# Kernel optimization log

Measured on AMD Instinct MI355X. Metric: run time of the kernel, lower is better.

Reference implementation:

```python
import jax, jax.numpy as jnp
import numpy as np

B, H, S, D = 16, 12, 1024, 64  # batch, heads, seq, head_dim (dim=768, num_head=12)


def setup_inputs() -> dict:
    key = jax.random.key(0)
    ks = jax.random.split(key, 9)
    sc = 1.0 / np.sqrt(D)
    return {
        "x": jax.random.normal(ks[0], (B, H, S, D), dtype=jnp.float32),
        "Wq": jax.random.normal(ks[1], (D, D), dtype=jnp.float32) * sc,
        "bq": jax.random.normal(ks[2], (D,), dtype=jnp.float32) * 0.02,
        "Wk": jax.random.normal(ks[3], (D, D), dtype=jnp.float32) * sc,
        "bk": jax.random.normal(ks[4], (D,), dtype=jnp.float32) * 0.02,
        "Wv": jax.random.normal(ks[5], (D, D), dtype=jnp.float32) * sc,
        "bv": jax.random.normal(ks[6], (D,), dtype=jnp.float32) * 0.02,
        "Wo": jax.random.normal(ks[7], (D, D), dtype=jnp.float32) * sc,
        "bo": jax.random.normal(ks[8], (D,), dtype=jnp.float32) * 0.02,
    }


def reference(x, Wq, bq, Wk, bk, Wv, bv, Wo, bo):
    # torch Linear: y = x @ W^T + b, applied to last dim (head_dim)
    q = jnp.einsum("bhsd,ed->bhse", x, Wq) + bq
    k = jnp.einsum("bhsd,ed->bhse", x, Wk) + bk
    v = jnp.einsum("bhsd,ed->bhse", x, Wv) + bv
    scores = jnp.einsum("bhqd,bhkd->bhqk", q, k) / jnp.sqrt(jnp.float32(q.shape[-1]))
    attn = jax.nn.softmax(scores, axis=-1)
    out = jnp.einsum("bhqk,bhkd->bhqd", attn, v)
    out = jnp.einsum("bhsd,ed->bhse", out, Wo) + bo
    return out
```

## Files before the change

kernel.cpp:

```cpp
#include <hip/hip_runtime.h>
#include <math.h>


typedef __bf16 bf16x8 __attribute__((ext_vector_type(8)));
typedef float  f32x4  __attribute__((ext_vector_type(4)));

#define MFMA(a, b, c) __builtin_amdgcn_mfma_f32_16x16x32_bf16((a), (b), (c), 0, 0, 0)

static constexpr int S = 1024;
static constexpr int PAD = 72;
static constexpr size_t NE = 196608ull * 64ull;
static constexpr float QSCALE = 0.125f * 1.4426950408889634f;

__device__ inline unsigned long long pack4bf(float a, float b, float c, float d) {
    union { __bf16 h[4]; unsigned long long u; } pk;
    pk.h[0] = (__bf16)a; pk.h[1] = (__bf16)b; pk.h[2] = (__bf16)c; pk.h[3] = (__bf16)d;
    return pk.u;
}

union frag_u { bf16x8 v; unsigned long long u[2]; };

__global__ void prep(const float* __restrict__ x,
                     const float* __restrict__ Wq, const float* __restrict__ Wk,
                     const float* __restrict__ Wv, const float* __restrict__ Wo,
                     __bf16* __restrict__ xb,
                     __bf16* __restrict__ wqb, __bf16* __restrict__ wkb,
                     __bf16* __restrict__ wvb, __bf16* __restrict__ wob)
{
    const int bid = blockIdx.x;
    if (bid < 6144) {
        size_t p = ((size_t)bid * 256 + threadIdx.x) * 8;
        float4 a = *(const float4*)(x + p);
        float4 b = *(const float4*)(x + p + 4);
        union { unsigned long long u64[2]; uint4 v; } pk;
        pk.u64[0] = pack4bf(a.x, a.y, a.z, a.w);
        pk.u64[1] = pack4bf(b.x, b.y, b.z, b.w);
        *(uint4*)(xb + p) = pk.v;
    } else {
        const int wb  = bid - 6144;
        const int grp = wb >> 2;
        const int p   = (((wb & 3) * 256) + threadIdx.x) * 4;
        if (grp == 3) {
            int e = p >> 6, s = p & 63;
            int h = s >> 5, qp = (s >> 3) & 3, tb = (s >> 2) & 1;
            int d0 = 32 * h + 16 * tb + 4 * qp;
            float4 v = *(const float4*)(Wo + e * 64 + d0);
            *(unsigned long long*)(wob + p) = pack4bf(v.x, v.y, v.z, v.w);
        } else {
            const float* src = (grp == 0) ? Wq : (grp == 1) ? Wk : Wv;
            __bf16*      dst = (grp == 0) ? wqb : (grp == 1) ? wkb : wvb;
            float4 v = *(const float4*)(src + p);
            *(unsigned long long*)(dst + p) = pack4bf(v.x, v.y, v.z, v.w);
        }
    }
}

__global__ __launch_bounds__(256, 2) void attn(
    const __bf16* __restrict__ xb,
    const __bf16* __restrict__ wqb, const __bf16* __restrict__ wkb,
    const __bf16* __restrict__ wvb, const __bf16* __restrict__ wob,
    const float* __restrict__ bq, const float* __restrict__ bk,
    const float* __restrict__ bv, const float* __restrict__ bo,
    float* __restrict__ out)
{
    __shared__ __align__(16) union {
        __bf16 xq[256][PAD];
        struct {
            __bf16 w[2][64][PAD];
            __bf16 k[64][PAD];
            __bf16 v[64][PAD];
            __bf16 xk[64][PAD];
        } m;
    } L;

    const int tid = threadIdx.x;
    const int w = tid >> 6, lane = tid & 63, m = lane & 15, quad = lane >> 4;
    const int bh = blockIdx.x;
    const int q0 = blockIdx.y * 256 + w * 64;

    const __bf16* xqbase = xb + ((size_t)bh * 1024 + blockIdx.y * 256) * 64;
    #pragma unroll
    for (int i = tid * 8, it = 0; it < 8; i += 2048, it++) {
        int r = i >> 6, c = i & 63;
        *(uint4*)&L.xq[r][c] = *(const uint4*)(xqbase + i);
    }
    __syncthreads();
    bf16x8 xqf[4][2];
    #pragma unroll
    for (int g = 0; g < 4; g++) {
        xqf[g][0] = *(const bf16x8*)&L.xq[w * 64 + g * 16 + m][quad * 8];
        xqf[g][1] = *(const bf16x8*)&L.xq[w * 64 + g * 16 + m][32 + quad * 8];
    }
    __syncthreads();
    #pragma unroll
    for (int et = 0; et < 4; et++) {
        bf16x8 wf0 = *(const bf16x8*)(wqb + (size_t)(et * 16 + m) * 64 + quad * 8);
        bf16x8 wf1 = *(const bf16x8*)(wqb + (size_t)(et * 16 + m) * 64 + 32 + quad * 8);
        float4 bias = *(const float4*)(bq + et * 16 + quad * 4);
        #pragma unroll
        for (int g = 0; g < 4; g++) {
            f32x4 acc = {0.f, 0.f, 0.f, 0.f};
            acc = MFMA(wf0, xqf[g][0], acc);
            acc = MFMA(wf1, xqf[g][1], acc);
            *(unsigned long long*)&L.xq[w * 64 + g * 16 + m][et * 16 + quad * 4] =
                pack4bf((acc[0] + bias.x) * QSCALE, (acc[1] + bias.y) * QSCALE,
                        (acc[2] + bias.z) * QSCALE, (acc[3] + bias.w) * QSCALE);
        }
    }
    __syncthreads();
    bf16x8 qf[4][2];
    #pragma unroll
    for (int g = 0; g < 4; g++) {
        qf[g][0] = *(const bf16x8*)&L.xq[w * 64 + g * 16 + m][quad * 8];
        qf[g][1] = *(const bf16x8*)&L.xq[w * 64 + g * 16 + m][32 + quad * 8];
    }
    __syncthreads();

    #pragma unroll
    for (int i = tid * 8, it = 0; it < 2; i += 2048, it++) {
        int r = i >> 6, c = i & 63;
        *(uint4*)&L.m.w[0][r][c] = *(const uint4*)(wkb + i);
        *(uint4*)&L.m.w[1][r][c] = *(const uint4*)(wvb + i);
    }
    float4 bkr[4];
    float  bvr[4];
    #pragma unroll
    for (int et = 0; et < 4; et++) {
        bkr[et] = *(const float4*)(bk + et * 16 + quad * 4);
        bvr[et] = bv[et * 16 + m];
    }

    f32x4 o[4][4];
    float lsum[4] = {0.f, 0.f, 0.f, 0.f};
    #pragma unroll
    for (int g = 0; g < 4; g++)
        #pragma unroll
        for (int n = 0; n < 4; n++) o[g][n] = {0.f, 0.f, 0.f, 0.f};

    const __bf16* xkey = xb + (size_t)bh * 1024 * 64;
    uint4 px0 = *(const uint4*)(xkey + tid * 8);
    uint4 px1 = *(const uint4*)(xkey + 2048 + tid * 8);

    const int p0 = 32 * (w >> 1) + 8 * quad + 4 * (w & 1);

    for (int kb = 0; kb < 16; kb++) {
        __syncthreads();
        {
            int i0 = tid * 8;
            int i1 = i0 + 2048;
            *(uint4*)&L.m.xk[i0 >> 6][i0 & 63] = px0;
            *(uint4*)&L.m.xk[i1 >> 6][i1 & 63] = px1;
        }
        __syncthreads();
        {
            bf16x8 xk0 = *(const bf16x8*)&L.m.xk[w * 16 + m][quad * 8];
            bf16x8 xk1 = *(const bf16x8*)&L.m.xk[w * 16 + m][32 + quad * 8];
            #pragma unroll
            for (int et = 0; et < 4; et++) {
                bf16x8 kw0 = *(const bf16x8*)&L.m.w[0][et * 16 + m][quad * 8];
                bf16x8 kw1 = *(const bf16x8*)&L.m.w[0][et * 16 + m][32 + quad * 8];
                f32x4 ka = {0.f, 0.f, 0.f, 0.f};
                ka = MFMA(kw0, xk0, ka);
                ka = MFMA(kw1, xk1, ka);
                *(unsigned long long*)&L.m.k[w * 16 + m][et * 16 + quad * 4] =
                    pack4bf(ka[0] + bkr[et].x, ka[1] + bkr[et].y,
                            ka[2] + bkr[et].z, ka[3] + bkr[et].w);
                bf16x8 vw0 = *(const bf16x8*)&L.m.w[1][et * 16 + m][quad * 8];
                bf16x8 vw1 = *(const bf16x8*)&L.m.w[1][et * 16 + m][32 + quad * 8];
                f32x4 va = {0.f, 0.f, 0.f, 0.f};
                va = MFMA(xk0, vw0, va);
                va = MFMA(xk1, vw1, va);
                *(unsigned long long*)&L.m.v[et * 16 + m][p0] =
                    pack4bf(va[0] + bvr[et], va[1] + bvr[et],
                            va[2] + bvr[et], va[3] + bvr[et]);
            }
        }
        if (kb < 15) {
            const __bf16* xn = xkey + (kb + 1) * 4096;
            px0 = *(const uint4*)(xn + tid * 8);
            px1 = *(const uint4*)(xn + 2048 + tid * 8);
        }
        __syncthreads();
        #pragma unroll
        for (int gp = 0; gp < 2; gp++) {
            frag_u pb[2][2];
            #pragma unroll
            for (int t = 0; t < 4; t++) {
                bf16x8 ka0 = *(const bf16x8*)&L.m.k[t * 16 + m][quad * 8];
                bf16x8 ka1 = *(const bf16x8*)&L.m.k[t * 16 + m][32 + quad * 8];
                #pragma unroll
                for (int gl = 0; gl < 2; gl++) {
                    const int g = gp * 2 + gl;
                    f32x4 acc = {0.f, 0.f, 0.f, 0.f};
                    acc = MFMA(ka0, qf[g][0], acc);
                    acc = MFMA(ka1, qf[g][1], acc);
                    float e0 = __builtin_amdgcn_exp2f(acc[0]);
                    float e1 = __builtin_amdgcn_exp2f(acc[1]);
                    float e2 = __builtin_amdgcn_exp2f(acc[2]);
                    float e3 = __builtin_amdgcn_exp2f(acc[3]);
                    lsum[g] += (e0 + e1) + (e2 + e3);
                    pb[gl][t >> 1].u[t & 1] = pack4bf(e0, e1, e2, e3);
                }
            }
            #pragma unroll
            for (int n = 0; n < 4; n++) {
                bf16x8 va0 = *(const bf16x8*)&L.m.v[n * 16 + m][quad * 8];
                bf16x8 va1 = *(const bf16x8*)&L.m.v[n * 16 + m][32 + quad * 8];
                #pragma unroll
                for (int gl = 0; gl < 2; gl++) {
                    const int g = gp * 2 + gl;
                    o[g][n] = MFMA(va0, pb[gl][0].v, o[g][n]);
                    o[g][n] = MFMA(va1, pb[gl][1].v, o[g][n]);
                }
            }
        }
    }

    #pragma unroll
    for (int g = 0; g < 4; g++) {
        lsum[g] += __shfl_xor(lsum[g], 16);
        lsum[g] += __shfl_xor(lsum[g], 32);
    }

    bf16x8 wf[4][2];
    #pragma unroll
    for (int et = 0; et < 4; et++) {
        wf[et][0] = *(const bf16x8*)(wob + (size_t)(et * 16 + m) * 64 + quad * 8);
        wf[et][1] = *(const bf16x8*)(wob + (size_t)(et * 16 + m) * 64 + 32 + quad * 8);
    }
    float biasr[4];
    #pragma unroll
    for (int et = 0; et < 4; et++) biasr[et] = bo[et * 16 + m];

    #pragma unroll
    for (int g = 0; g < 4; g++) {
        const float inv = 1.f / lsum[g];
        frag_u af0, af1;
        af0.u[0] = pack4bf(o[g][0][0] * inv, o[g][0][1] * inv, o[g][0][2] * inv, o[g][0][3] * inv);
        af0.u[1] = pack4bf(o[g][1][0] * inv, o[g][1][1] * inv, o[g][1][2] * inv, o[g][1][3] * inv);
        af1.u[0] = pack4bf(o[g][2][0] * inv, o[g][2][1] * inv, o[g][2][2] * inv, o[g][2][3] * inv);
        af1.u[1] = pack4bf(o[g][3][0] * inv, o[g][3][1] * inv, o[g][3][2] * inv, o[g][3][3] * inv);
        #pragma unroll
        for (int et = 0; et < 4; et++) {
            f32x4 acc = {0.f, 0.f, 0.f, 0.f};
            acc = MFMA(af0.v, wf[et][0], acc);
            acc = MFMA(af1.v, wf[et][1], acc);
            #pragma unroll
            for (int r = 0; r < 4; r++) {
                size_t row = (size_t)bh * S + q0 + g * 16 + quad * 4 + r;
                out[row * 64 + et * 16 + m] = acc[r] + biasr[et];
            }
        }
    }
}

extern "C" void kernel_launch(void* const* d_in, const int* in_sizes, int n_in,
                              void* d_out, int out_size, void* d_ws, size_t ws_size,
                              hipStream_t stream) {
    const float* x  = (const float*)d_in[0];
    const float* Wq = (const float*)d_in[1];
    const float* bq = (const float*)d_in[2];
    const float* Wk = (const float*)d_in[3];
    const float* bk = (const float*)d_in[4];
    const float* Wv = (const float*)d_in[5];
    const float* bv = (const float*)d_in[6];
    const float* Wo = (const float*)d_in[7];
    const float* bo = (const float*)d_in[8];
    float* out = (float*)d_out;

    __bf16* xb  = (__bf16*)d_ws;
    __bf16* wob = xb + NE;
    __bf16* wqb = wob + 4096;
    __bf16* wkb = wqb + 4096;
    __bf16* wvb = wkb + 4096;

    prep<<<6160, 256, 0, stream>>>(x, Wq, Wk, Wv, Wo, xb, wqb, wkb, wvb, wob);
    attn<<<dim3(192, 4), 256, 0, stream>>>(xb, wqb, wkb, wvb, wob,
                                           bq, bk, bv, bo, out);
}
```

Before: 195.9 us.

## Fuse fp32-to-bf16 conversion into attention kernel and drop prep pass

Removes the separate prep kernel that converted x and the weights to bf16 in workspace; the attention kernel now reads fp32 inputs directly and packs to bf16 in registers. Key-block x rows are loaded straight into MFMA fragments instead of via an LDS staging buffer with register prefetch, which frees LDS and one barrier per iteration. Launch bounds are raised to allow 4 blocks per CU. The cost is doubled global read bytes for x (fp32, re-read by 4 query blocks) and the loss of the explicit next-block prefetch overlap.

```diff
diff --git a/kernel.cpp b/kernel.cpp
--- a/kernel.cpp
+++ b/kernel.cpp
@@ -9,7 +9,6 @@
 
 static constexpr int S = 1024;
 static constexpr int PAD = 72;
-static constexpr size_t NE = 196608ull * 64ull;
 static constexpr float QSCALE = 0.125f * 1.4426950408889634f;
 
 __device__ inline unsigned long long pack4bf(float a, float b, float c, float d) {
@@ -20,47 +19,12 @@
 
 union frag_u { bf16x8 v; unsigned long long u[2]; };
 
-__global__ void prep(const float* __restrict__ x,
-                     const float* __restrict__ Wq, const float* __restrict__ Wk,
-                     const float* __restrict__ Wv, const float* __restrict__ Wo,
-                     __bf16* __restrict__ xb,
-                     __bf16* __restrict__ wqb, __bf16* __restrict__ wkb,
-                     __bf16* __restrict__ wvb, __bf16* __restrict__ wob)
-{
-    const int bid = blockIdx.x;
-    if (bid < 6144) {
-        size_t p = ((size_t)bid * 256 + threadIdx.x) * 8;
-        float4 a = *(const float4*)(x + p);
-        float4 b = *(const float4*)(x + p + 4);
-        union { unsigned long long u64[2]; uint4 v; } pk;
-        pk.u64[0] = pack4bf(a.x, a.y, a.z, a.w);
-        pk.u64[1] = pack4bf(b.x, b.y, b.z, b.w);
-        *(uint4*)(xb + p) = pk.v;
-    } else {
-        const int wb  = bid - 6144;
-        const int grp = wb >> 2;
-        const int p   = (((wb & 3) * 256) + threadIdx.x) * 4;
-        if (grp == 3) {
-            int e = p >> 6, s = p & 63;
-            int h = s >> 5, qp = (s >> 3) & 3, tb = (s >> 2) & 1;
-            int d0 = 32 * h + 16 * tb + 4 * qp;
-            float4 v = *(const float4*)(Wo + e * 64 + d0);
-            *(unsigned long long*)(wob + p) = pack4bf(v.x, v.y, v.z, v.w);
-        } else {
-            const float* src = (grp == 0) ? Wq : (grp == 1) ? Wk : Wv;
-            __bf16*      dst = (grp == 0) ? wqb : (grp == 1) ? wkb : wvb;
-            float4 v = *(const float4*)(src + p);
-            *(unsigned long long*)(dst + p) = pack4bf(v.x, v.y, v.z, v.w);
-        }
-    }
-}
-
-__global__ __launch_bounds__(256, 2) void attn(
-    const __bf16* __restrict__ xb,
-    const __bf16* __restrict__ wqb, const __bf16* __restrict__ wkb,
-    const __bf16* __restrict__ wvb, const __bf16* __restrict__ wob,
-    const float* __restrict__ bq, const float* __restrict__ bk,
-    const float* __restrict__ bv, const float* __restrict__ bo,
+__global__ __launch_bounds__(256, 4) void attn(
+    const float* __restrict__ x,
+    const float* __restrict__ Wq, const float* __restrict__ bq,
+    const float* __restrict__ Wk, const float* __restrict__ bk,
+    const float* __restrict__ Wv, const float* __restrict__ bv,
+    const float* __restrict__ Wo, const float* __restrict__ bo,
     float* __restrict__ out)
 {
     __shared__ __align__(16) union {
@@ -69,7 +33,6 @@
             __bf16 w[2][64][PAD];
             __bf16 k[64][PAD];
             __bf16 v[64][PAD];
-            __bf16 xk[64][PAD];
         } m;
     } L;
 
@@ -78,11 +41,12 @@
     const int bh = blockIdx.x;
     const int q0 = blockIdx.y * 256 + w * 64;
 
-    const __bf16* xqbase = xb + ((size_t)bh * 1024 + blockIdx.y * 256) * 64;
-    #pragma unroll
-    for (int i = tid * 8, it = 0; it < 8; i += 2048, it++) {
+    const float* xq32 = x + ((size_t)bh * 1024 + blockIdx.y * 256) * 64;
+    #pragma unroll
+    for (int i = tid * 4; i < 16384; i += 1024) {
+        float4 v = *(const float4*)(xq32 + i);
         int r = i >> 6, c = i & 63;
-        *(uint4*)&L.xq[r][c] = *(const uint4*)(xqbase + i);
+        *(unsigned long long*)&L.xq[r][c] = pack4bf(v.x, v.y, v.z, v.w);
     }
     __syncthreads();
     bf16x8 xqf[4][2];
@@ -92,16 +56,25 @@
         xqf[g][1] = *(const bf16x8*)&L.xq[w * 64 + g * 16 + m][32 + quad * 8];
     }
     __syncthreads();
+
     #pragma unroll
     for (int et = 0; et < 4; et++) {
-        bf16x8 wf0 = *(const bf16x8*)(wqb + (size_t)(et * 16 + m) * 64 + quad * 8);
-        bf16x8 wf1 = *(const bf16x8*)(wqb + (size_t)(et * 16 + m) * 64 + 32 + quad * 8);
+        const float* wqrow = Wq + (size_t)(et * 16 + m) * 64;
+        float4 a0 = *(const float4*)(wqrow + quad * 8);
+        float4 a1 = *(const float4*)(wqrow + quad * 8 + 4);
+        float4 a2 = *(const float4*)(wqrow + 32 + quad * 8);
+        float4 a3 = *(const float4*)(wqrow + 36 + quad * 8);
+        frag_u wf0, wf1;
+        wf0.u[0] = pack4bf(a0.x, a0.y, a0.z, a0.w);
+        wf0.u[1] = pack4bf(a1.x, a1.y, a1.z, a1.w);
+        wf1.u[0] = pack4bf(a2.x, a2.y, a2.z, a2.w);
+        wf1.u[1] = pack4bf(a3.x, a3.y, a3.z, a3.w);
         float4 bias = *(const float4*)(bq + et * 16 + quad * 4);
         #pragma unroll
         for (int g = 0; g < 4; g++) {
             f32x4 acc = {0.f, 0.f, 0.f, 0.f};
-            acc = MFMA(wf0, xqf[g][0], acc);
-            acc = MFMA(wf1, xqf[g][1], acc);
+            acc = MFMA(wf0.v, xqf[g][0], acc);
+            acc = MFMA(wf1.v, xqf[g][1], acc);
             *(unsigned long long*)&L.xq[w * 64 + g * 16 + m][et * 16 + quad * 4] =
                 pack4bf((acc[0] + bias.x) * QSCALE, (acc[1] + bias.y) * QSCALE,
                         (acc[2] + bias.z) * QSCALE, (acc[3] + bias.w) * QSCALE);
@@ -117,10 +90,12 @@
     __syncthreads();
 
     #pragma unroll
-    for (int i = tid * 8, it = 0; it < 2; i += 2048, it++) {
+    for (int i = tid * 4; i < 4096; i += 1024) {
         int r = i >> 6, c = i & 63;
-        *(uint4*)&L.m.w[0][r][c] = *(const uint4*)(wkb + i);
-        *(uint4*)&L.m.w[1][r][c] = *(const uint4*)(wvb + i);
+        float4 a = *(const float4*)(Wk + i);
+        *(unsigned long long*)&L.m.w[0][r][c] = pack4bf(a.x, a.y, a.z, a.w);
+        float4 b = *(const float4*)(Wv + i);
+        *(unsigned long long*)&L.m.w[1][r][c] = pack4bf(b.x, b.y, b.z, b.w);
     }
     float4 bkr[4];
     float  bvr[4];
@@ -137,48 +112,41 @@
         #pragma unroll
         for (int n = 0; n < 4; n++) o[g][n] = {0.f, 0.f, 0.f, 0.f};
 
-    const __bf16* xkey = xb + (size_t)bh * 1024 * 64;
-    uint4 px0 = *(const uint4*)(xkey + tid * 8);
-    uint4 px1 = *(const uint4*)(xkey + 2048 + tid * 8);
-
+    const float* xk32 = x + (size_t)bh * 1024 * 64;
     const int p0 = 32 * (w >> 1) + 8 * quad + 4 * (w & 1);
 
     for (int kb = 0; kb < 16; kb++) {
         __syncthreads();
         {
-            int i0 = tid * 8;
-            int i1 = i0 + 2048;
-            *(uint4*)&L.m.xk[i0 >> 6][i0 & 63] = px0;
-            *(uint4*)&L.m.xk[i1 >> 6][i1 & 63] = px1;
-        }
-        __syncthreads();
-        {
-            bf16x8 xk0 = *(const bf16x8*)&L.m.xk[w * 16 + m][quad * 8];
-            bf16x8 xk1 = *(const bf16x8*)&L.m.xk[w * 16 + m][32 + quad * 8];
+            const float* xrow = xk32 + (size_t)(kb * 64 + w * 16 + m) * 64;
+            float4 a0 = *(const float4*)(xrow + quad * 8);
+            float4 a1 = *(const float4*)(xrow + quad * 8 + 4);
+            float4 a2 = *(const float4*)(xrow + 32 + quad * 8);
+            float4 a3 = *(const float4*)(xrow + 36 + quad * 8);
+            frag_u xk0, xk1;
+            xk0.u[0] = pack4bf(a0.x, a0.y, a0.z, a0.w);
+            xk0.u[1] = pack4bf(a1.x, a1.y, a1.z, a1.w);
+            xk1.u[0] = pack4bf(a2.x, a2.y, a2.z, a2.w);
+            xk1.u[1] = pack4bf(a3.x, a3.y, a3.z, a3.w);
             #pragma unroll
             for (int et = 0; et < 4; et++) {
                 bf16x8 kw0 = *(const bf16x8*)&L.m.w[0][et * 16 + m][quad * 8];
                 bf16x8 kw1 = *(const bf16x8*)&L.m.w[0][et * 16 + m][32 + quad * 8];
                 f32x4 ka = {0.f, 0.f, 0.f, 0.f};
-                ka = MFMA(kw0, xk0, ka);
-                ka = MFMA(kw1, xk1, ka);
+                ka = MFMA(kw0, xk0.v, ka);
+                ka = MFMA(kw1, xk1.v, ka);
                 *(unsigned long long*)&L.m.k[w * 16 + m][et * 16 + quad * 4] =
                     pack4bf(ka[0] + bkr[et].x, ka[1] + bkr[et].y,
                             ka[2] + bkr[et].z, ka[3] + bkr[et].w);
                 bf16x8 vw0 = *(const bf16x8*)&L.m.w[1][et * 16 + m][quad * 8];
                 bf16x8 vw1 = *(const bf16x8*)&L.m.w[1][et * 16 + m][32 + quad * 8];
                 f32x4 va = {0.f, 0.f, 0.f, 0.f};
-                va = MFMA(xk0, vw0, va);
-                va = MFMA(xk1, vw1, va);
+                va = MFMA(xk0.v, vw0, va);
+                va = MFMA(xk1.v, vw1, va);
                 *(unsigned long long*)&L.m.v[et * 16 + m][p0] =
                     pack4bf(va[0] + bvr[et], va[1] + bvr[et],
                             va[2] + bvr[et], va[3] + bvr[et]);
             }
-        }
-        if (kb < 15) {
-            const __bf16* xn = xkey + (kb + 1) * 4096;
-            px0 = *(const uint4*)(xn + tid * 8);
-            px1 = *(const uint4*)(xn + 2048 + tid * 8);
         }
         __syncthreads();
         #pragma unroll
@@ -225,8 +193,18 @@
     bf16x8 wf[4][2];
     #pragma unroll
     for (int et = 0; et < 4; et++) {
-        wf[et][0] = *(const bf16x8*)(wob + (size_t)(et * 16 + m) * 64 + quad * 8);
-        wf[et][1] = *(const bf16x8*)(wob + (size_t)(et * 16 + m) * 64 + 32 + quad * 8);
+        const float* worow = Wo + (size_t)(et * 16 + m) * 64;
+        float4 c0 = *(const float4*)(worow + 4 * quad);
+        float4 c1 = *(const float4*)(worow + 16 + 4 * quad);
+        float4 c2 = *(const float4*)(worow + 32 + 4 * quad);
+        float4 c3 = *(const float4*)(worow + 48 + 4 * quad);
+        frag_u f0, f1;
+        f0.u[0] = pack4bf(c0.x, c0.y, c0.z, c0.w);
+        f0.u[1] = pack4bf(c1.x, c1.y, c1.z, c1.w);
+        f1.u[0] = pack4bf(c2.x, c2.y, c2.z, c2.w);
+        f1.u[1] = pack4bf(c3.x, c3.y, c3.z, c3.w);
+        wf[et][0] = f0.v;
+        wf[et][1] = f1.v;
     }
     float biasr[4];
     #pragma unroll
@@ -268,13 +246,5 @@
     const float* bo = (const float*)d_in[8];
     float* out = (float*)d_out;
 
-    __bf16* xb  = (__bf16*)d_ws;
-    __bf16* wob = xb + NE;
-    __bf16* wqb = wob + 4096;
-    __bf16* wkb = wqb + 4096;
-    __bf16* wvb = wkb + 4096;
-
-    prep<<<6160, 256, 0, stream>>>(x, Wq, Wk, Wv, Wo, xb, wqb, wkb, wvb, wob);
-    attn<<<dim3(192, 4), 256, 0, stream>>>(xb, wqb, wkb, wvb, wob,
-                                           bq, bk, bv, bo, out);
+    attn<<<dim3(192, 4), 256, 0, stream>>>(x, Wq, bq, Wk, bk, Wv, bv, Wo, bo, out);
 }
```

Result: slower. 423.0 us (+115.9%).

## Load key-block x fragments directly into registers and pre-swizzle K/V weights

Applied to the files above, without the earlier changes.

Drops the LDS staging of each 64-row x key block. Each lane now loads its MFMA fragment straight from global memory, prefetched one block ahead, which removes one barrier per iteration. The K/V weights are stored once in a fragment-ordered LDS layout so each lane reads them contiguously, and two prologue barriers are removed. The attention MFMA section is also wrapped in s_setprio to favour compute waves. The cost is more scattered global loads per lane and a separate LDS array that is no longer unioned with the Q buffer.

```diff
diff --git a/kernel.cpp b/kernel.cpp
--- a/kernel.cpp
+++ b/kernel.cpp
@@ -66,12 +66,11 @@
     __shared__ __align__(16) union {
         __bf16 xq[256][PAD];
         struct {
-            __bf16 w[2][64][PAD];
             __bf16 k[64][PAD];
             __bf16 v[64][PAD];
-            __bf16 xk[64][PAD];
         } m;
     } L;
+    __shared__ __align__(16) __bf16 lw[2][8][64][8];
 
     const int tid = threadIdx.x;
     const int w = tid >> 6, lane = tid & 63, m = lane & 15, quad = lane >> 4;
@@ -84,14 +83,23 @@
         int r = i >> 6, c = i & 63;
         *(uint4*)&L.xq[r][c] = *(const uint4*)(xqbase + i);
     }
+    #pragma unroll
+    for (int c = tid; c < 1024; c += 256) {
+        int mtx = c >> 9, rest = c & 511;
+        int fe = rest >> 6, ln = rest & 63;
+        int mm = ln & 15, qq = ln >> 4;
+        int et = fe >> 1, half = fe & 1;
+        const __bf16* src = (mtx ? wvb : wkb) + (size_t)(et * 16 + mm) * 64 + half * 32 + qq * 8;
+        *(uint4*)&lw[mtx][fe][ln][0] = *(const uint4*)src;
+    }
     __syncthreads();
+
     bf16x8 xqf[4][2];
     #pragma unroll
     for (int g = 0; g < 4; g++) {
         xqf[g][0] = *(const bf16x8*)&L.xq[w * 64 + g * 16 + m][quad * 8];
         xqf[g][1] = *(const bf16x8*)&L.xq[w * 64 + g * 16 + m][32 + quad * 8];
     }
-    __syncthreads();
     #pragma unroll
     for (int et = 0; et < 4; et++) {
         bf16x8 wf0 = *(const bf16x8*)(wqb + (size_t)(et * 16 + m) * 64 + quad * 8);
@@ -107,7 +115,6 @@
                         (acc[2] + bias.z) * QSCALE, (acc[3] + bias.w) * QSCALE);
         }
     }
-    __syncthreads();
     bf16x8 qf[4][2];
     #pragma unroll
     for (int g = 0; g < 4; g++) {
@@ -116,12 +123,6 @@
     }
     __syncthreads();
 
-    #pragma unroll
-    for (int i = tid * 8, it = 0; it < 2; i += 2048, it++) {
-        int r = i >> 6, c = i & 63;
-        *(uint4*)&L.m.w[0][r][c] = *(const uint4*)(wkb + i);
-        *(uint4*)&L.m.w[1][r][c] = *(const uint4*)(wvb + i);
-    }
     float4 bkr[4];
     float  bvr[4];
     #pragma unroll
@@ -138,49 +139,43 @@
         for (int n = 0; n < 4; n++) o[g][n] = {0.f, 0.f, 0.f, 0.f};
 
     const __bf16* xkey = xb + (size_t)bh * 1024 * 64;
-    uint4 px0 = *(const uint4*)(xkey + tid * 8);
-    uint4 px1 = *(const uint4*)(xkey + 2048 + tid * 8);
-
     const int p0 = 32 * (w >> 1) + 8 * quad + 4 * (w & 1);
+
+    bf16x8 xk0 = *(const bf16x8*)(xkey + (size_t)(w * 16 + m) * 64 + quad * 8);
+    bf16x8 xk1 = *(const bf16x8*)(xkey + (size_t)(w * 16 + m) * 64 + 32 + quad * 8);
 
     for (int kb = 0; kb < 16; kb++) {
         __syncthreads();
-        {
-            int i0 = tid * 8;
-            int i1 = i0 + 2048;
-            *(uint4*)&L.m.xk[i0 >> 6][i0 & 63] = px0;
-            *(uint4*)&L.m.xk[i1 >> 6][i1 & 63] = px1;
+
+        bf16x8 nx0, nx1;
+        if (kb < 15) {
+            const __bf16* xrow = xkey + (size_t)((kb + 1) * 64 + w * 16 + m) * 64;
+            nx0 = *(const bf16x8*)(xrow + quad * 8);
+            nx1 = *(const bf16x8*)(xrow + 32 + quad * 8);
+        }
+
+        #pragma unroll
+        for (int et = 0; et < 4; et++) {
+            bf16x8 kw0 = *(const bf16x8*)&lw[0][et * 2 + 0][lane][0];
+            bf16x8 kw1 = *(const bf16x8*)&lw[0][et * 2 + 1][lane][0];
+            f32x4 ka = {0.f, 0.f, 0.f, 0.f};
+            ka = MFMA(kw0, xk0, ka);
+            ka = MFMA(kw1, xk1, ka);
+            *(unsigned long long*)&L.m.k[w * 16 + m][et * 16 + quad * 4] =
+                pack4bf(ka[0] + bkr[et].x, ka[1] + bkr[et].y,
+                        ka[2] + bkr[et].z, ka[3] + bkr[et].w);
+            bf16x8 vw0 = *(const bf16x8*)&lw[1][et * 2 + 0][lane][0];
+            bf16x8 vw1 = *(const bf16x8*)&lw[1][et * 2 + 1][lane][0];
+            f32x4 va = {0.f, 0.f, 0.f, 0.f};
+            va = MFMA(xk0, vw0, va);
+            va = MFMA(xk1, vw1, va);
+            *(unsigned long long*)&L.m.v[et * 16 + m][p0] =
+                pack4bf(va[0] + bvr[et], va[1] + bvr[et],
+                        va[2] + bvr[et], va[3] + bvr[et]);
         }
         __syncthreads();
-        {
-            bf16x8 xk0 = *(const bf16x8*)&L.m.xk[w * 16 + m][quad * 8];
-            bf16x8 xk1 = *(const bf16x8*)&L.m.xk[w * 16 + m][32 + quad * 8];
-            #pragma unroll
-            for (int et = 0; et < 4; et++) {
-                bf16x8 kw0 = *(const bf16x8*)&L.m.w[0][et * 16 + m][quad * 8];
-                bf16x8 kw1 = *(const bf16x8*)&L.m.w[0][et * 16 + m][32 + quad * 8];
-                f32x4 ka = {0.f, 0.f, 0.f, 0.f};
-                ka = MFMA(kw0, xk0, ka);
-                ka = MFMA(kw1, xk1, ka);
-                *(unsigned long long*)&L.m.k[w * 16 + m][et * 16 + quad * 4] =
-                    pack4bf(ka[0] + bkr[et].x, ka[1] + bkr[et].y,
-                            ka[2] + bkr[et].z, ka[3] + bkr[et].w);
-                bf16x8 vw0 = *(const bf16x8*)&L.m.w[1][et * 16 + m][quad * 8];
-                bf16x8 vw1 = *(const bf16x8*)&L.m.w[1][et * 16 + m][32 + quad * 8];
-                f32x4 va = {0.f, 0.f, 0.f, 0.f};
-                va = MFMA(xk0, vw0, va);
-                va = MFMA(xk1, vw1, va);
-                *(unsigned long long*)&L.m.v[et * 16 + m][p0] =
-                    pack4bf(va[0] + bvr[et], va[1] + bvr[et],
-                            va[2] + bvr[et], va[3] + bvr[et]);
-            }
-        }
-        if (kb < 15) {
-            const __bf16* xn = xkey + (kb + 1) * 4096;
-            px0 = *(const uint4*)(xn + tid * 8);
-            px1 = *(const uint4*)(xn + 2048 + tid * 8);
-        }
-        __syncthreads();
+
+        __builtin_amdgcn_s_setprio(1);
         #pragma unroll
         for (int gp = 0; gp < 2; gp++) {
             frag_u pb[2][2];
@@ -214,6 +209,9 @@
                 }
             }
         }
+        __builtin_amdgcn_s_setprio(0);
+
+        xk0 = nx0; xk1 = nx1;
     }
 
     #pragma unroll
```

After: 195.3 us. Within noise of the previous version (-0.3%).
